# Kernel tuning notes

Measured on AMD Instinct MI355X. Metric: run time of the kernel, lower is better.

## Reference

```python
import jax, jax.numpy as jnp
import numpy as np


def setup_inputs() -> dict:
    key = jax.random.key(0)
    ks = jax.random.split(key, 5)
    T, B, C, H, K = 2048, 8, 1024, 16, 7
    s = 1.0 / np.sqrt(C)
    return {
        "x": jax.random.normal(ks[0], (T, B, C), dtype=jnp.float32),
        "w_weight": jax.random.normal(ks[1], (H * K, C), dtype=jnp.float32) * s,
        "glu_w": jax.random.normal(ks[2], (2 * H, C), dtype=jnp.float32) * s,
        "glu_b": jnp.zeros((2 * H,), dtype=jnp.float32),
        "out_w": jax.random.normal(ks[3], (C, C), dtype=jnp.float32) * s,
        "out_b": jnp.zeros((C,), dtype=jnp.float32),
        "padding_l": 6,
    }


def reference(x, w_weight, glu_w, glu_b, out_w, out_b, padding_l):
    # x: (T, B, C) in TBC format
    T, B, C = x.shape
    H = glu_w.shape[0] // 2
    K = w_weight.shape[0] // H
    R = C // H  # channels per head

    # GLU gate: C -> 2H, split last dim, a * sigmoid(b)  -> (T, B, H)
    g = (x @ glu_w.T + glu_b).reshape(T, B, H, 2)
    gate = g[..., 0] * jax.nn.sigmoid(g[..., 1])

    # per-position per-head kernel weights, softmax over K -> (T, B, H, K)
    w = jax.nn.softmax((x @ w_weight.T).reshape(T, B, H, K), axis=-1)

    # depthwise dynamic conv: out[t] = sum_k w[t,k] * x_pad[t + k]
    xh = x.reshape(T, B, H, R)
    xp = jnp.pad(xh, ((padding_l, K - 1 - padding_l), (0, 0), (0, 0), (0, 0)))
    conv = jnp.zeros_like(xh)
    for k in range(K):  # K is small & static; avoids (B,H,T,K,R) unfold blowup
        conv = conv + w[..., k:k + 1] * jax.lax.dynamic_slice_in_dim(xp, k, T, axis=0)

    # gate per head, merge heads, output projection
    out = (conv * gate[..., None]).reshape(T, B, C)
    return out @ out_w.T + out_b
```

## Files before the change

kernel.cpp:

```cpp
#include <hip/hip_runtime.h>
#include <hip/hip_bf16.h>
#include <stdint.h>

#define T_DIM 2048
#define B_DIM 8
#define C_DIM 1024
#define H_DIM 16
#define K_DIM 7
#define M_DIM (T_DIM * B_DIM)
#define NLOG 144

typedef __attribute__((ext_vector_type(8))) short short8;
typedef __attribute__((ext_vector_type(4))) float floatx4;

__device__ __forceinline__ ushort f2bf(float f) {
    __hip_bfloat16 h = __float2bfloat16(f);
    return *(ushort*)&h;
}

#define S_W  ((size_t)112 * C_DIM)
#define S_G  ((size_t)32 * C_DIM)
#define S_O  ((size_t)C_DIM * C_DIM)
#define S_WG (S_W + S_G)
#define S_CVT (S_WG + S_O)

__global__ __launch_bounds__(256) void cvt_w_kernel(
    const float* __restrict__ w_weight, const float* __restrict__ glu_w,
    const float* __restrict__ out_w,
    ushort* __restrict__ wb, ushort* __restrict__ Wb)
{
    size_t gid = ((size_t)blockIdx.x * 256 + threadIdx.x) * 4;
    const float* src; ushort* dst; size_t off;
    if (gid < S_W)            { src = w_weight; dst = wb;       off = gid; }
    else if (gid < S_WG)      { src = glu_w;    dst = wb + S_W; off = gid - S_W; }
    else                      { src = out_w;    dst = Wb;       off = gid - S_WG; }
    float4 v = *(const float4*)(src + off);
    ushort4 o; o.x = f2bf(v.x); o.y = f2bf(v.y); o.z = f2bf(v.z); o.w = f2bf(v.w);
    *(ushort4*)(dst + off) = o;
}

__global__ __launch_bounds__(256) void fused_logits_conv(
    const float* __restrict__ x,
    const ushort* __restrict__ wb,
    const float* __restrict__ glu_b,
    const int* __restrict__ padding_l_,
    ushort* __restrict__ y)
{
    __shared__ float part[4][16][NLOG];
    __shared__ float wk[16][H_DIM][K_DIM];
    __shared__ float gg[16][H_DIM];

    const int tid = threadIdx.x;
    const int wave = tid >> 6, lane = tid & 63;
    const int fr = lane & 15, q = lane >> 4;
    const int m0 = blockIdx.x * 16;

    floatx4 acc[9];
#pragma unroll
    for (int j = 0; j < 9; ++j) acc[j] = (floatx4){0.f, 0.f, 0.f, 0.f};

    const float* arow  = x  + (size_t)(m0 + fr) * C_DIM + wave * 256 + q * 8;
    const ushort* brow = wb + (size_t)fr * C_DIM        + wave * 256 + q * 8;

#pragma unroll
    for (int it = 0; it < 8; ++it) {
        float4 v0 = *(const float4*)(arow + it * 32);
        float4 v1 = *(const float4*)(arow + it * 32 + 4);
        short8 a;
        a[0] = (short)f2bf(v0.x); a[1] = (short)f2bf(v0.y);
        a[2] = (short)f2bf(v0.z); a[3] = (short)f2bf(v0.w);
        a[4] = (short)f2bf(v1.x); a[5] = (short)f2bf(v1.y);
        a[6] = (short)f2bf(v1.z); a[7] = (short)f2bf(v1.w);
#pragma unroll
        for (int j = 0; j < 9; ++j) {
            short8 b = *(const short8*)(brow + (size_t)j * 16 * C_DIM + it * 32);
            acc[j] = __builtin_amdgcn_mfma_f32_16x16x32_bf16(a, b, acc[j], 0, 0, 0);
        }
    }
#pragma unroll
    for (int j = 0; j < 9; ++j)
#pragma unroll
        for (int r = 0; r < 4; ++r)
            part[wave][q * 4 + r][j * 16 + fr] = acc[j][r];
    __syncthreads();

    {
        const int row = tid >> 4, h = tid & 15;
        float l[K_DIM];
        float mx = -1e30f;
#pragma unroll
        for (int k = 0; k < K_DIM; ++k) {
            float s = part[0][row][h * K_DIM + k] + part[1][row][h * K_DIM + k]
                    + part[2][row][h * K_DIM + k] + part[3][row][h * K_DIM + k];
            l[k] = s; mx = fmaxf(mx, s);
        }
        float s = 0.f;
#pragma unroll
        for (int k = 0; k < K_DIM; ++k) { l[k] = __expf(l[k] - mx); s += l[k]; }
        float inv = 1.f / s;
#pragma unroll
        for (int k = 0; k < K_DIM; ++k) wk[row][h][k] = l[k] * inv;
        float ga = part[0][row][112 + 2 * h] + part[1][row][112 + 2 * h]
                 + part[2][row][112 + 2 * h] + part[3][row][112 + 2 * h] + glu_b[2 * h];
        float gb = part[0][row][113 + 2 * h] + part[1][row][113 + 2 * h]
                 + part[2][row][113 + 2 * h] + part[3][row][113 + 2 * h] + glu_b[2 * h + 1];
        gg[row][h] = ga * (1.f / (1.f + __expf(-gb)));
    }
    __syncthreads();

    const int pad = *padding_l_;
    const int c0 = lane * 16;
    const int h = lane >> 2;
    for (int rr = wave; rr < 16; rr += 4) {
        const int m = m0 + rr;
        const int t = m >> 3;
        float av[16];
#pragma unroll
        for (int i = 0; i < 16; ++i) av[i] = 0.f;
#pragma unroll
        for (int k = 0; k < K_DIM; ++k) {
            int ts = t + k - pad;
            if (ts < 0 || ts >= T_DIM) continue;
            float wv = wk[rr][h][k];
            const float4* xp = (const float4*)(x + ((size_t)m + 8 * (k - pad)) * C_DIM + c0);
            float4 u0 = xp[0], u1 = xp[1], u2 = xp[2], u3 = xp[3];
            av[0]  += wv * u0.x; av[1]  += wv * u0.y; av[2]  += wv * u0.z; av[3]  += wv * u0.w;
            av[4]  += wv * u1.x; av[5]  += wv * u1.y; av[6]  += wv * u1.z; av[7]  += wv * u1.w;
            av[8]  += wv * u2.x; av[9]  += wv * u2.y; av[10] += wv * u2.z; av[11] += wv * u2.w;
            av[12] += wv * u3.x; av[13] += wv * u3.y; av[14] += wv * u3.z; av[15] += wv * u3.w;
        }
        float g = gg[rr][h];
        uint32_t o[8];
#pragma unroll
        for (int i = 0; i < 8; ++i)
            o[i] = (uint32_t)f2bf(av[2 * i] * g) | ((uint32_t)f2bf(av[2 * i + 1] * g) << 16);
        uint4* yr = (uint4*)(y + (size_t)m * C_DIM + c0);
        yr[0] = (uint4){o[0], o[1], o[2], o[3]};
        yr[1] = (uint4){o[4], o[5], o[6], o[7]};
    }
}

__global__ __launch_bounds__(256) void out_gemm(
    const ushort* __restrict__ y,
    const ushort* __restrict__ Wb,
    const float* __restrict__ bias,
    float* __restrict__ out)
{
    __shared__ __align__(16) ushort As[128 * 64];
    __shared__ __align__(16) ushort Bs[128 * 64];

    const int bm = blockIdx.x & 127;
    const int bn = blockIdx.x >> 7;
    const int m0 = bm * 128, n0 = bn * 128;
    const int tid = threadIdx.x;
    const int lane = tid & 63, wave = tid >> 6;
    const int wm = (wave >> 1) * 64, wn = (wave & 1) * 64;
    const int fr = lane & 15, q = lane >> 4;

    floatx4 acc[4][4];
#pragma unroll
    for (int i = 0; i < 4; ++i)
#pragma unroll
        for (int j = 0; j < 4; ++j) acc[i][j] = (floatx4){0.f, 0.f, 0.f, 0.f};

    for (int k0 = 0; k0 < C_DIM; k0 += 64) {
        __syncthreads();
#pragma unroll
        for (int j = 0; j < 4; ++j) {
            int idx = j * 256 + tid;
            int r = idx >> 3, cl = idx & 7;
            int ch = cl ^ (r & 7);
            const ushort* ga = y + (size_t)(m0 + r) * C_DIM + k0 + ch * 8;
            __builtin_amdgcn_global_load_lds(
                (const __attribute__((address_space(1))) void*)ga,
                (__attribute__((address_space(3))) void*)(As + idx * 8), 16, 0, 0);
            const ushort* gb = Wb + (size_t)(n0 + r) * C_DIM + k0 + ch * 8;
            __builtin_amdgcn_global_load_lds(
                (const __attribute__((address_space(1))) void*)gb,
                (__attribute__((address_space(3))) void*)(Bs + idx * 8), 16, 0, 0);
        }
        __syncthreads();

#pragma unroll
        for (int s = 0; s < 64; s += 32) {
            const int cbase = (s >> 3) + q;
            short8 a[4], b[4];
#pragma unroll
            for (int i = 0; i < 4; ++i) {
                int r = wm + i * 16 + fr;
                a[i] = *(const short8*)(As + r * 64 + ((cbase ^ (r & 7)) * 8));
            }
#pragma unroll
            for (int j = 0; j < 4; ++j) {
                int r = wn + j * 16 + fr;
                b[j] = *(const short8*)(Bs + r * 64 + ((cbase ^ (r & 7)) * 8));
            }
#pragma unroll
            for (int i = 0; i < 4; ++i)
#pragma unroll
                for (int j = 0; j < 4; ++j)
                    acc[i][j] = __builtin_amdgcn_mfma_f32_16x16x32_bf16(a[i], b[j], acc[i][j], 0, 0, 0);
        }
    }

#pragma unroll
    for (int j = 0; j < 4; ++j) {
        int n = n0 + wn + j * 16 + fr;
        float bv = bias[n];
#pragma unroll
        for (int i = 0; i < 4; ++i) {
#pragma unroll
            for (int r = 0; r < 4; ++r) {
                int m = m0 + wm + i * 16 + q * 4 + r;
                out[(size_t)m * C_DIM + n] = acc[i][j][r] + bv;
            }
        }
    }
}

extern "C" void kernel_launch(void* const* d_in, const int* in_sizes, int n_in,
                              void* d_out, int out_size, void* d_ws, size_t ws_size,
                              hipStream_t stream) {
    const float* x        = (const float*)d_in[0];
    const float* w_weight = (const float*)d_in[1];
    const float* glu_w    = (const float*)d_in[2];
    const float* glu_b    = (const float*)d_in[3];
    const float* out_w    = (const float*)d_in[4];
    const float* out_b    = (const float*)d_in[5];
    const int* padding_l  = (const int*)d_in[6];
    float* out = (float*)d_out;

    char* ws = (char*)d_ws;
    ushort* y  = (ushort*)ws;
    ushort* wb = y + (size_t)M_DIM * C_DIM;
    ushort* Wb = wb + S_WG;

    cvt_w_kernel<<<S_CVT / 4 / 256, 256, 0, stream>>>(w_weight, glu_w, out_w, wb, Wb);
    fused_logits_conv<<<M_DIM / 16, 256, 0, stream>>>(x, wb, glu_b, padding_l, y);
    out_gemm<<<(M_DIM / 128) * (C_DIM / 128), 256, 0, stream>>>(y, Wb, out_b, out);
}
```

Measured before the change: 244.6 us.

## Split fused logits/conv into separate kernels with LDS-staged weight tiles

Splits the fused logits+conv kernel in two. The logits kernel now gives each wave its own 16 rows (64 rows per block) across the full K dimension, so the cross-wave partial-sum reduction goes away. Weight tiles are double-buffered into LDS with global_load_lds. The softmax weights and gate go to a workspace buffer, and a separate conv kernel reads them with a block-index swizzle. The out_gemm block order is also swapped so blocks sharing the same M rows run together. The cost is an extra launch and a workspace round-trip for the per-row weights.

```diff
diff --git a/kernel.cpp b/kernel.cpp
--- a/kernel.cpp
+++ b/kernel.cpp
@@ -9,6 +9,7 @@
 #define K_DIM 7
 #define M_DIM (T_DIM * B_DIM)
 #define NLOG 144
+#define CW_STRIDE 128
 
 typedef __attribute__((ext_vector_type(8))) short short8;
 typedef __attribute__((ext_vector_type(4))) float floatx4;
@@ -39,105 +40,140 @@
     *(ushort4*)(dst + off) = o;
 }
 
-__global__ __launch_bounds__(256) void fused_logits_conv(
+__global__ __launch_bounds__(256) void logits_kernel(
     const float* __restrict__ x,
     const ushort* __restrict__ wb,
     const float* __restrict__ glu_b,
-    const int* __restrict__ padding_l_,
-    ushort* __restrict__ y)
-{
-    __shared__ float part[4][16][NLOG];
-    __shared__ float wk[16][H_DIM][K_DIM];
-    __shared__ float gg[16][H_DIM];
+    float* __restrict__ cw)
+{
+    __shared__ __align__(16) ushort Bs[2][144 * 32];
+    __shared__ float lsm[64][NLOG];
 
     const int tid = threadIdx.x;
     const int wave = tid >> 6, lane = tid & 63;
     const int fr = lane & 15, q = lane >> 4;
-    const int m0 = blockIdx.x * 16;
+    const int m0 = blockIdx.x * 64;
+    const int mrow = m0 + wave * 16 + fr;
 
     floatx4 acc[9];
 #pragma unroll
     for (int j = 0; j < 9; ++j) acc[j] = (floatx4){0.f, 0.f, 0.f, 0.f};
 
-    const float* arow  = x  + (size_t)(m0 + fr) * C_DIM + wave * 256 + q * 8;
-    const ushort* brow = wb + (size_t)fr * C_DIM        + wave * 256 + q * 8;
-
-#pragma unroll
-    for (int it = 0; it < 8; ++it) {
-        float4 v0 = *(const float4*)(arow + it * 32);
-        float4 v1 = *(const float4*)(arow + it * 32 + 4);
+    const float* arow = x + (size_t)mrow * C_DIM + q * 8;
+
+    for (int i = tid; i < 576; i += 256) {
+        int r = i >> 2, ch = i & 3;
+        __builtin_amdgcn_global_load_lds(
+            (const __attribute__((address_space(1))) void*)(wb + (size_t)r * C_DIM + ch * 8),
+            (__attribute__((address_space(3))) void*)(&Bs[0][0] + i * 8), 16, 0, 0);
+    }
+    float4 a0 = *(const float4*)(arow);
+    float4 a1 = *(const float4*)(arow + 4);
+    __syncthreads();
+
+    for (int kc = 0; kc < 32; ++kc) {
+        const int buf = kc & 1;
+        if (kc < 31) {
+            const ushort* wsrc = wb + (kc + 1) * 32;
+            for (int i = tid; i < 576; i += 256) {
+                int r = i >> 2, ch = i & 3;
+                __builtin_amdgcn_global_load_lds(
+                    (const __attribute__((address_space(1))) void*)(wsrc + (size_t)r * C_DIM + ch * 8),
+                    (__attribute__((address_space(3))) void*)(&Bs[buf ^ 1][0] + i * 8), 16, 0, 0);
+            }
+        }
         short8 a;
-        a[0] = (short)f2bf(v0.x); a[1] = (short)f2bf(v0.y);
-        a[2] = (short)f2bf(v0.z); a[3] = (short)f2bf(v0.w);
-        a[4] = (short)f2bf(v1.x); a[5] = (short)f2bf(v1.y);
-        a[6] = (short)f2bf(v1.z); a[7] = (short)f2bf(v1.w);
+        a[0] = (short)f2bf(a0.x); a[1] = (short)f2bf(a0.y);
+        a[2] = (short)f2bf(a0.z); a[3] = (short)f2bf(a0.w);
+        a[4] = (short)f2bf(a1.x); a[5] = (short)f2bf(a1.y);
+        a[6] = (short)f2bf(a1.z); a[7] = (short)f2bf(a1.w);
+        if (kc < 31) {
+            a0 = *(const float4*)(arow + (kc + 1) * 32);
+            a1 = *(const float4*)(arow + (kc + 1) * 32 + 4);
+        }
 #pragma unroll
         for (int j = 0; j < 9; ++j) {
-            short8 b = *(const short8*)(brow + (size_t)j * 16 * C_DIM + it * 32);
+            short8 b = *(const short8*)(&Bs[buf][0] + ((j * 16 + fr) * 4 + q) * 8);
             acc[j] = __builtin_amdgcn_mfma_f32_16x16x32_bf16(a, b, acc[j], 0, 0, 0);
         }
-    }
+        __syncthreads();
+    }
+
 #pragma unroll
     for (int j = 0; j < 9; ++j)
 #pragma unroll
         for (int r = 0; r < 4; ++r)
-            part[wave][q * 4 + r][j * 16 + fr] = acc[j][r];
+            lsm[wave * 16 + q * 4 + r][j * 16 + fr] = acc[j][r];
     __syncthreads();
 
     {
-        const int row = tid >> 4, h = tid & 15;
-        float l[K_DIM];
-        float mx = -1e30f;
-#pragma unroll
-        for (int k = 0; k < K_DIM; ++k) {
-            float s = part[0][row][h * K_DIM + k] + part[1][row][h * K_DIM + k]
-                    + part[2][row][h * K_DIM + k] + part[3][row][h * K_DIM + k];
-            l[k] = s; mx = fmaxf(mx, s);
-        }
-        float s = 0.f;
-#pragma unroll
-        for (int k = 0; k < K_DIM; ++k) { l[k] = __expf(l[k] - mx); s += l[k]; }
-        float inv = 1.f / s;
-#pragma unroll
-        for (int k = 0; k < K_DIM; ++k) wk[row][h][k] = l[k] * inv;
-        float ga = part[0][row][112 + 2 * h] + part[1][row][112 + 2 * h]
-                 + part[2][row][112 + 2 * h] + part[3][row][112 + 2 * h] + glu_b[2 * h];
-        float gb = part[0][row][113 + 2 * h] + part[1][row][113 + 2 * h]
-                 + part[2][row][113 + 2 * h] + part[3][row][113 + 2 * h] + glu_b[2 * h + 1];
-        gg[row][h] = ga * (1.f / (1.f + __expf(-gb)));
-    }
-    __syncthreads();
-
+        const int row = tid >> 2;
+        const int hbase = (tid & 3) * 4;
+        float* crow = cw + (size_t)(m0 + row) * CW_STRIDE;
+#pragma unroll
+        for (int hh = 0; hh < 4; ++hh) {
+            const int h = hbase + hh;
+            float l[K_DIM];
+            float mx = -1e30f;
+#pragma unroll
+            for (int k = 0; k < K_DIM; ++k) { l[k] = lsm[row][h * K_DIM + k]; mx = fmaxf(mx, l[k]); }
+            float s = 0.f;
+#pragma unroll
+            for (int k = 0; k < K_DIM; ++k) { l[k] = __expf(l[k] - mx); s += l[k]; }
+            float inv = 1.f / s;
+#pragma unroll
+            for (int k = 0; k < K_DIM; ++k) crow[h * K_DIM + k] = l[k] * inv;
+            float ga = lsm[row][112 + 2 * h] + glu_b[2 * h];
+            float gb = lsm[row][113 + 2 * h] + glu_b[2 * h + 1];
+            crow[112 + h] = ga * (1.f / (1.f + __expf(-gb)));
+        }
+    }
+}
+
+__global__ __launch_bounds__(256) void conv_kernel(
+    const float* __restrict__ x,
+    const float* __restrict__ cw,
+    const int* __restrict__ padding_l_,
+    ushort* __restrict__ y)
+{
+    const int lb = (blockIdx.x & 7) * 512 + (blockIdx.x >> 3);
+    const int wave = threadIdx.x >> 6, lane = threadIdx.x & 63;
+    const int m = lb * 4 + wave;
+    const int t = m >> 3;
     const int pad = *padding_l_;
+    const int h = lane >> 2;
+
+    const float* crow = cw + (size_t)m * CW_STRIDE;
+    float wt[K_DIM];
+#pragma unroll
+    for (int k = 0; k < K_DIM; ++k) wt[k] = crow[h * K_DIM + k];
+    const float g = crow[112 + h];
+
     const int c0 = lane * 16;
-    const int h = lane >> 2;
-    for (int rr = wave; rr < 16; rr += 4) {
-        const int m = m0 + rr;
-        const int t = m >> 3;
-        float av[16];
-#pragma unroll
-        for (int i = 0; i < 16; ++i) av[i] = 0.f;
-#pragma unroll
-        for (int k = 0; k < K_DIM; ++k) {
-            int ts = t + k - pad;
-            if (ts < 0 || ts >= T_DIM) continue;
-            float wv = wk[rr][h][k];
-            const float4* xp = (const float4*)(x + ((size_t)m + 8 * (k - pad)) * C_DIM + c0);
-            float4 u0 = xp[0], u1 = xp[1], u2 = xp[2], u3 = xp[3];
-            av[0]  += wv * u0.x; av[1]  += wv * u0.y; av[2]  += wv * u0.z; av[3]  += wv * u0.w;
-            av[4]  += wv * u1.x; av[5]  += wv * u1.y; av[6]  += wv * u1.z; av[7]  += wv * u1.w;
-            av[8]  += wv * u2.x; av[9]  += wv * u2.y; av[10] += wv * u2.z; av[11] += wv * u2.w;
-            av[12] += wv * u3.x; av[13] += wv * u3.y; av[14] += wv * u3.z; av[15] += wv * u3.w;
-        }
-        float g = gg[rr][h];
-        uint32_t o[8];
-#pragma unroll
-        for (int i = 0; i < 8; ++i)
-            o[i] = (uint32_t)f2bf(av[2 * i] * g) | ((uint32_t)f2bf(av[2 * i + 1] * g) << 16);
-        uint4* yr = (uint4*)(y + (size_t)m * C_DIM + c0);
-        yr[0] = (uint4){o[0], o[1], o[2], o[3]};
-        yr[1] = (uint4){o[4], o[5], o[6], o[7]};
-    }
+    float av[16];
+#pragma unroll
+    for (int i = 0; i < 16; ++i) av[i] = 0.f;
+
+#pragma unroll
+    for (int k = 0; k < K_DIM; ++k) {
+        int ts = t + k - pad;
+        if (ts < 0 || ts >= T_DIM) continue;
+        float wv = wt[k];
+        const float4* xp = (const float4*)(x + ((size_t)m + 8 * (k - pad)) * C_DIM + c0);
+        float4 u0 = xp[0], u1 = xp[1], u2 = xp[2], u3 = xp[3];
+        av[0]  += wv * u0.x; av[1]  += wv * u0.y; av[2]  += wv * u0.z; av[3]  += wv * u0.w;
+        av[4]  += wv * u1.x; av[5]  += wv * u1.y; av[6]  += wv * u1.z; av[7]  += wv * u1.w;
+        av[8]  += wv * u2.x; av[9]  += wv * u2.y; av[10] += wv * u2.z; av[11] += wv * u2.w;
+        av[12] += wv * u3.x; av[13] += wv * u3.y; av[14] += wv * u3.z; av[15] += wv * u3.w;
+    }
+
+    uint32_t o[8];
+#pragma unroll
+    for (int i = 0; i < 8; ++i)
+        o[i] = (uint32_t)f2bf(av[2 * i] * g) | ((uint32_t)f2bf(av[2 * i + 1] * g) << 16);
+    uint4* yr = (uint4*)(y + (size_t)m * C_DIM + c0);
+    yr[0] = (uint4){o[0], o[1], o[2], o[3]};
+    yr[1] = (uint4){o[4], o[5], o[6], o[7]};
 }
 
 __global__ __launch_bounds__(256) void out_gemm(
@@ -149,8 +185,8 @@
     __shared__ __align__(16) ushort As[128 * 64];
     __shared__ __align__(16) ushort Bs[128 * 64];
 
-    const int bm = blockIdx.x & 127;
-    const int bn = blockIdx.x >> 7;
+    const int bn = blockIdx.x & 7;
+    const int bm = blockIdx.x >> 3;
     const int m0 = bm * 128, n0 = bn * 128;
     const int tid = threadIdx.x;
     const int lane = tid & 63, wave = tid >> 6;
@@ -234,8 +270,10 @@
     ushort* y  = (ushort*)ws;
     ushort* wb = y + (size_t)M_DIM * C_DIM;
     ushort* Wb = wb + S_WG;
+    float* cwp = (float*)(Wb + S_O);
 
     cvt_w_kernel<<<S_CVT / 4 / 256, 256, 0, stream>>>(w_weight, glu_w, out_w, wb, Wb);
-    fused_logits_conv<<<M_DIM / 16, 256, 0, stream>>>(x, wb, glu_b, padding_l, y);
+    logits_kernel<<<M_DIM / 64, 256, 0, stream>>>(x, wb, glu_b, cwp);
+    conv_kernel<<<M_DIM / 4, 256, 0, stream>>>(x, cwp, padding_l, y);
     out_gemm<<<(M_DIM / 128) * (C_DIM / 128), 256, 0, stream>>>(y, Wb, out_b, out);
 }
```

Result: faster. 229.8 us (-6.1%).

## Split fused logits/conv kernel into separate logits and conv kernels

Applied to the files above, without the earlier changes.

Splits the fused kernel in two. The first computes the softmax conv weights and GLU gates and writes them to a workspace buffer; the second, launched with a finer grid of one row per wave and a swizzled block order, does the depthwise conv. It also reduces the logits loop unroll with a launch_bounds occupancy hint and reorders out_gemm blocks so the N tiles of one M tile are adjacent. The aim is better occupancy and L2 locality, at the cost of an extra launch and a global round-trip for the weights.

```diff
diff --git a/kernel.cpp b/kernel.cpp
--- a/kernel.cpp
+++ b/kernel.cpp
@@ -9,6 +9,7 @@
 #define K_DIM 7
 #define M_DIM (T_DIM * B_DIM)
 #define NLOG 144
+#define CW_STRIDE 128
 
 typedef __attribute__((ext_vector_type(8))) short short8;
 typedef __attribute__((ext_vector_type(4))) float floatx4;
@@ -39,16 +40,13 @@
     *(ushort4*)(dst + off) = o;
 }
 
-__global__ __launch_bounds__(256) void fused_logits_conv(
+__global__ __launch_bounds__(256, 4) void logits_kernel(
     const float* __restrict__ x,
     const ushort* __restrict__ wb,
     const float* __restrict__ glu_b,
-    const int* __restrict__ padding_l_,
-    ushort* __restrict__ y)
+    float* __restrict__ cw)
 {
     __shared__ float part[4][16][NLOG];
-    __shared__ float wk[16][H_DIM][K_DIM];
-    __shared__ float gg[16][H_DIM];
 
     const int tid = threadIdx.x;
     const int wave = tid >> 6, lane = tid & 63;
@@ -62,10 +60,10 @@
     const float* arow  = x  + (size_t)(m0 + fr) * C_DIM + wave * 256 + q * 8;
     const ushort* brow = wb + (size_t)fr * C_DIM        + wave * 256 + q * 8;
 
-#pragma unroll
-    for (int it = 0; it < 8; ++it) {
-        float4 v0 = *(const float4*)(arow + it * 32);
-        float4 v1 = *(const float4*)(arow + it * 32 + 4);
+#pragma unroll 2
+    for (int kc = 0; kc < 8; ++kc) {
+        float4 v0 = *(const float4*)(arow + kc * 32);
+        float4 v1 = *(const float4*)(arow + kc * 32 + 4);
         short8 a;
         a[0] = (short)f2bf(v0.x); a[1] = (short)f2bf(v0.y);
         a[2] = (short)f2bf(v0.z); a[3] = (short)f2bf(v0.w);
@@ -73,10 +71,11 @@
         a[6] = (short)f2bf(v1.z); a[7] = (short)f2bf(v1.w);
 #pragma unroll
         for (int j = 0; j < 9; ++j) {
-            short8 b = *(const short8*)(brow + (size_t)j * 16 * C_DIM + it * 32);
+            short8 b = *(const short8*)(brow + (size_t)j * 16 * C_DIM + kc * 32);
             acc[j] = __builtin_amdgcn_mfma_f32_16x16x32_bf16(a, b, acc[j], 0, 0, 0);
         }
     }
+
 #pragma unroll
     for (int j = 0; j < 9; ++j)
 #pragma unroll
@@ -86,6 +85,7 @@
 
     {
         const int row = tid >> 4, h = tid & 15;
+        float* crow = cw + (size_t)(m0 + row) * CW_STRIDE;
         float l[K_DIM];
         float mx = -1e30f;
 #pragma unroll
@@ -99,45 +99,59 @@
         for (int k = 0; k < K_DIM; ++k) { l[k] = __expf(l[k] - mx); s += l[k]; }
         float inv = 1.f / s;
 #pragma unroll
-        for (int k = 0; k < K_DIM; ++k) wk[row][h][k] = l[k] * inv;
+        for (int k = 0; k < K_DIM; ++k) crow[h * K_DIM + k] = l[k] * inv;
         float ga = part[0][row][112 + 2 * h] + part[1][row][112 + 2 * h]
                  + part[2][row][112 + 2 * h] + part[3][row][112 + 2 * h] + glu_b[2 * h];
         float gb = part[0][row][113 + 2 * h] + part[1][row][113 + 2 * h]
                  + part[2][row][113 + 2 * h] + part[3][row][113 + 2 * h] + glu_b[2 * h + 1];
-        gg[row][h] = ga * (1.f / (1.f + __expf(-gb)));
-    }
-    __syncthreads();
-
+        crow[112 + h] = ga * (1.f / (1.f + __expf(-gb)));
+    }
+}
+
+__global__ __launch_bounds__(256) void conv_kernel(
+    const float* __restrict__ x,
+    const float* __restrict__ cw,
+    const int* __restrict__ padding_l_,
+    ushort* __restrict__ y)
+{
+    const int lb = (blockIdx.x & 7) * 512 + (blockIdx.x >> 3);
+    const int wave = threadIdx.x >> 6, lane = threadIdx.x & 63;
+    const int m = lb * 4 + wave;
+    const int t = m >> 3;
     const int pad = *padding_l_;
+    const int h = lane >> 2;
+
+    const float* crow = cw + (size_t)m * CW_STRIDE;
+    float wt[K_DIM];
+#pragma unroll
+    for (int k = 0; k < K_DIM; ++k) wt[k] = crow[h * K_DIM + k];
+    const float g = crow[112 + h];
+
     const int c0 = lane * 16;
-    const int h = lane >> 2;
-    for (int rr = wave; rr < 16; rr += 4) {
-        const int m = m0 + rr;
-        const int t = m >> 3;
-        float av[16];
-#pragma unroll
-        for (int i = 0; i < 16; ++i) av[i] = 0.f;
-#pragma unroll
-        for (int k = 0; k < K_DIM; ++k) {
-            int ts = t + k - pad;
-            if (ts < 0 || ts >= T_DIM) continue;
-            float wv = wk[rr][h][k];
-            const float4* xp = (const float4*)(x + ((size_t)m + 8 * (k - pad)) * C_DIM + c0);
-            float4 u0 = xp[0], u1 = xp[1], u2 = xp[2], u3 = xp[3];
-            av[0]  += wv * u0.x; av[1]  += wv * u0.y; av[2]  += wv * u0.z; av[3]  += wv * u0.w;
-            av[4]  += wv * u1.x; av[5]  += wv * u1.y; av[6]  += wv * u1.z; av[7]  += wv * u1.w;
-            av[8]  += wv * u2.x; av[9]  += wv * u2.y; av[10] += wv * u2.z; av[11] += wv * u2.w;
-            av[12] += wv * u3.x; av[13] += wv * u3.y; av[14] += wv * u3.z; av[15] += wv * u3.w;
-        }
-        float g = gg[rr][h];
-        uint32_t o[8];
-#pragma unroll
-        for (int i = 0; i < 8; ++i)
-            o[i] = (uint32_t)f2bf(av[2 * i] * g) | ((uint32_t)f2bf(av[2 * i + 1] * g) << 16);
-        uint4* yr = (uint4*)(y + (size_t)m * C_DIM + c0);
-        yr[0] = (uint4){o[0], o[1], o[2], o[3]};
-        yr[1] = (uint4){o[4], o[5], o[6], o[7]};
-    }
+    float av[16];
+#pragma unroll
+    for (int i = 0; i < 16; ++i) av[i] = 0.f;
+
+#pragma unroll
+    for (int k = 0; k < K_DIM; ++k) {
+        int ts = t + k - pad;
+        if (ts < 0 || ts >= T_DIM) continue;
+        float wv = wt[k];
+        const float4* xp = (const float4*)(x + ((size_t)m + 8 * (k - pad)) * C_DIM + c0);
+        float4 u0 = xp[0], u1 = xp[1], u2 = xp[2], u3 = xp[3];
+        av[0]  += wv * u0.x; av[1]  += wv * u0.y; av[2]  += wv * u0.z; av[3]  += wv * u0.w;
+        av[4]  += wv * u1.x; av[5]  += wv * u1.y; av[6]  += wv * u1.z; av[7]  += wv * u1.w;
+        av[8]  += wv * u2.x; av[9]  += wv * u2.y; av[10] += wv * u2.z; av[11] += wv * u2.w;
+        av[12] += wv * u3.x; av[13] += wv * u3.y; av[14] += wv * u3.z; av[15] += wv * u3.w;
+    }
+
+    uint32_t o[8];
+#pragma unroll
+    for (int i = 0; i < 8; ++i)
+        o[i] = (uint32_t)f2bf(av[2 * i] * g) | ((uint32_t)f2bf(av[2 * i + 1] * g) << 16);
+    uint4* yr = (uint4*)(y + (size_t)m * C_DIM + c0);
+    yr[0] = (uint4){o[0], o[1], o[2], o[3]};
+    yr[1] = (uint4){o[4], o[5], o[6], o[7]};
 }
 
 __global__ __launch_bounds__(256) void out_gemm(
@@ -149,8 +163,8 @@
     __shared__ __align__(16) ushort As[128 * 64];
     __shared__ __align__(16) ushort Bs[128 * 64];
 
-    const int bm = blockIdx.x & 127;
-    const int bn = blockIdx.x >> 7;
+    const int bn = blockIdx.x & 7;
+    const int bm = blockIdx.x >> 3;
     const int m0 = bm * 128, n0 = bn * 128;
     const int tid = threadIdx.x;
     const int lane = tid & 63, wave = tid >> 6;
@@ -234,8 +248,10 @@
     ushort* y  = (ushort*)ws;
     ushort* wb = y + (size_t)M_DIM * C_DIM;
     ushort* Wb = wb + S_WG;
+    float* cwp = (float*)(Wb + S_O);
 
     cvt_w_kernel<<<S_CVT / 4 / 256, 256, 0, stream>>>(w_weight, glu_w, out_w, wb, Wb);
-    fused_logits_conv<<<M_DIM / 16, 256, 0, stream>>>(x, wb, glu_b, padding_l, y);
+    logits_kernel<<<M_DIM / 16, 256, 0, stream>>>(x, wb, glu_b, cwp);
+    conv_kernel<<<M_DIM / 4, 256, 0, stream>>>(x, cwp, padding_l, y);
     out_gemm<<<(M_DIM / 128) * (C_DIM / 128), 256, 0, stream>>>(y, Wb, out_b, out);
 }
```

New measurement: 233.4 us. 4.6% less time.
